# Kernel optimization log

Measured on AMD Instinct MI355X. Metric: run time of the kernel, lower is better.

Reference implementation:

```python
import jax, jax.numpy as jnp
import numpy as np

N = 8192          # rays
S = 128           # steps per ray (cfg.n_steps_fixed)
POS_BANDS = 10    # positional-encoding bands for positions
VD_BANDS = 4      # bands for view directions (default in _encode_viewdir)
EARLY_STOP_T = 1e-4


def pos_enc(x, num_bands):
    """[..., 3] -> [..., 3 + 2*3*num_bands], interleaved [x, sin(f*x), cos(f*x), ...]."""
    parts = [x]
    for i in range(num_bands):  # small fixed loop over frequency bands
        f = jnp.asarray(2.0 ** i, dtype=x.dtype)
        parts.append(jnp.sin(f * x))
        parts.append(jnp.cos(f * x))
    return jnp.concatenate(parts, axis=-1)


def setup_inputs() -> dict:
    key = jax.random.key(0)
    ks = jax.random.split(key, 10)
    orig = 0.1 * jax.random.normal(ks[0], (N, 3), jnp.float32)
    dirs = jax.random.normal(ks[1], (N, 3), jnp.float32)
    dirs = dirs / (jnp.linalg.norm(dirs, axis=-1, keepdims=True) + 1e-8)
    tmin = 0.5 + 0.5 * jax.random.uniform(ks[2], (N,), jnp.float32)
    tmax = tmin + 1.0 + jax.random.uniform(ks[3], (N,), jnp.float32)
    d_enc = 3 + 2 * 3 * POS_BANDS          # 63
    d_vd = 3 + 2 * 3 * VD_BANDS            # 27
    hid, feat = 64, 15
    W1 = jax.random.normal(ks[4], (d_enc, hid), jnp.float32) / np.sqrt(d_enc)
    b1 = jnp.zeros((hid,), jnp.float32)
    W2 = jax.random.normal(ks[5], (hid, 1 + feat), jnp.float32) / np.sqrt(hid)
    b2 = jnp.zeros((1 + feat,), jnp.float32)
    V1 = jax.random.normal(ks[6], (feat + d_vd, hid), jnp.float32) / np.sqrt(feat + d_vd)
    c1 = jnp.zeros((hid,), jnp.float32)
    V2 = jax.random.normal(ks[7], (hid, 3), jnp.float32) / np.sqrt(hid)
    c2 = jnp.zeros((3,), jnp.float32)
    return {"orig": orig, "dirs": dirs, "tmin": tmin, "tmax": tmax,
            "W1": W1, "b1": b1, "W2": W2, "b2": b2,
            "V1": V1, "c1": c1, "V2": V2, "c2": c2}


def reference(orig, dirs, tmin, tmax, W1, b1, W2, b2, V1, c1, V2, c2):
    # --- fixed-step sampling ---
    t_uniform = jnp.linspace(0.0, 1.0, S, dtype=jnp.float32)          # [S]
    t = tmin[:, None] + t_uniform[None, :] * (tmax - tmin)[:, None]   # [N, S]
    dt = jnp.mean(tmax - tmin) / S                                    # scalar step size

    # --- positions and encoder ---
    pos = orig[:, None, :] + dirs[:, None, :] * t[..., None]          # [N, S, 3]
    enc = pos_enc(pos, POS_BANDS)                                     # [N, S, 63]

    # --- field MLP: sigma + rgb features ---
    h = jax.nn.relu(enc @ W1 + b1)                                    # [N, S, 64]
    out = h @ W2 + b2                                                 # [N, S, 16]
    sigma = jax.nn.relu(out[..., 0])                                  # [N, S]
    rgb_feat = out[..., 1:]                                           # [N, S, 15]

    # --- rgb head with view-direction PE ---
    vd = dirs / (jnp.linalg.norm(dirs, axis=-1, keepdims=True) + 1e-8)
    vd_enc = pos_enc(vd, VD_BANDS)                                    # [N, 27]
    vd_enc = jnp.broadcast_to(vd_enc[:, None, :], (rgb_feat.shape[0], S, vd_enc.shape[-1]))
    rgb_in = jnp.concatenate([rgb_feat, vd_enc], axis=-1)             # [N, S, 42]
    rgb_steps = jax.nn.sigmoid(jax.nn.relu(rgb_in @ V1 + c1) @ V2 + c2)  # [N, S, 3]

    # --- alpha compositing with early stop (dense-masked equivalent) ---
    alpha = 1.0 - jnp.exp(-sigma * dt)                                # [N, S]
    one_minus = 1.0 - alpha
    T_excl = jnp.concatenate(
        [jnp.ones_like(alpha[:, :1]), jnp.cumprod(one_minus, axis=1)[:, :-1]], axis=1
    )                                                                 # transmittance before each step
    active = T_excl > EARLY_STOP_T                                    # ray still marching
    weights = T_excl * alpha * active                                 # [N, S]
    rgb_out = jnp.sum(weights[..., None] * rgb_steps, axis=1)         # [N, 3]
    T_out = jnp.prod(jnp.where(active, one_minus, 1.0), axis=1)       # final transmittance at stop
    return rgb_out, T_out
```

## Files before the change

kernel.cpp:

```cpp
#include <hip/hip_runtime.h>
#include <hip/hip_bf16.h>

#define NRAYS 8192
#define SAMP  128
#define DVD   27
#define NFEAT 15

typedef float  f32x4  __attribute__((ext_vector_type(4)));
typedef short  short8 __attribute__((ext_vector_type(8)));
typedef unsigned int u32x2 __attribute__((ext_vector_type(2)));
typedef unsigned int u32x4 __attribute__((ext_vector_type(4)));

#define GVC_OFF  16896
#define IMG_CHUNKS 1056

static __device__ __forceinline__ int XB(int row, int cb) {
    return row * 128 + (cb ^ ((row & 7) << 4));
}
static __device__ __forceinline__ int XS(int row, int k) {
    return row * 64 + (k ^ ((row & 7) << 3));
}

static __device__ __forceinline__ void stbf(short* p, float x) {
    union { unsigned u; struct { short lo, hi; } s; } v;
    v.u = __float_as_uint(x) + 0x8000u;
    *p = v.s.hi;
}
static __device__ __forceinline__ float bf2f(short s) {
    return __uint_as_float(((unsigned)(unsigned short)s) << 16);
}
static __device__ __forceinline__ unsigned pk2bf(float lo, float hi) {
    unsigned r;
    asm("v_cvt_pk_bf16_f32 %0, %1, %2" : "=v"(r) : "v"(lo), "v"(hi));
    return r;
}
static __device__ __forceinline__ float sin_fast(float x) {
    float r = x * 0.15915494309189535f;
    r = r - floorf(r);
    return __builtin_amdgcn_sinf(r);
}
static __device__ __forceinline__ float cos_fast(float x) {
    float r = x * 0.15915494309189535f;
    r = r - floorf(r);
    return __builtin_amdgcn_cosf(r);
}
static __device__ __forceinline__ float sigm(float x) {
    return 1.0f / (1.0f + __expf(-x));
}

static __device__ __forceinline__ int kmap(int r) {
    if (r == 0) return 30;
    if (r == 1) return 31;
    if (r == 2) return 62;
    const int q = r - 3, i = q / 6, c = q - 6 * i;
    return (i < 5 ? 6 * i : 32 + 6 * (i - 5)) + c;
}

__global__ void __launch_bounds__(256)
prep_kernel(const float* __restrict__ W1, const float* __restrict__ b1,
            const float* __restrict__ W2, const float* __restrict__ b2,
            const float* __restrict__ V1, const float* __restrict__ c1,
            const float* __restrict__ V2, short* __restrict__ img,
            float* __restrict__ gvc) {
    const int g = blockIdx.x * 256 + threadIdx.x;
    if (g < 4032) {
        const int r = g >> 6, n = g & 63;
        const int prow = (n & 3) * 16 + (n >> 2);
        stbf(&img[XS(prow, kmap(r))], W1[g]);
    } else if (g < 4096) {
        const int n = g - 4032;
        const int prow = (n & 3) * 16 + (n >> 2);
        stbf(&img[XS(prow, 63)], b1[n]);
    } else if (g < 8192) {
        const int i = g - 4096;
        const int k = i >> 6, n = i & 63;
        const int prow = (n & 3) * 16 + (n >> 2);
        float a = 0.0f;
        #pragma unroll
        for (int j = 0; j < 15; j++) a += W2[k * 16 + 1 + j] * V1[j * 64 + n];
        stbf(&img[4096 + XS(prow, k)], a);
    } else if (g < 8256) {
        const int k = g - 8192;
        stbf(&img[8192 + k], W2[k * 16]);
    } else if (g < 8448) {
        const int i = g - 8256, c = i >> 6, k = i & 63;
        stbf(&img[8192 + 64 + c * 64 + k], V2[k * 3 + c]);
    } else if (g < 8512) {
        const int n = g - 8448;
        float a = c1[n];
        #pragma unroll
        for (int j = 0; j < 15; j++) a += b2[1 + j] * V1[j * 64 + n];
        gvc[n] = a;
    }
}

#define SMEM_BYTES 38400

__global__ void __launch_bounds__(256, 4)
march_kernel(const float* __restrict__ orig,
             const float* __restrict__ dirs,
             const float* __restrict__ tmin,
             const float* __restrict__ tmax,
             const float* __restrict__ b2,
             const float* __restrict__ c2,
             const float* __restrict__ V1,
             const short* __restrict__ img,
             const float* __restrict__ gvc,
             float* __restrict__ out) {
    __shared__ __align__(16) char smem[SMEM_BYTES];
    char*  const sEc   = smem;
    char*  const sW1tc = smem + 16384;
    char*  const sCtc  = smem + 24576;
    short* const sSm   = (short*)(smem + 32768);
    float* const sOm   = (float*)(smem + 33280);
    short* const sRgb  = (short*)(smem + 35328);
    float* const sVde  = (float*)(smem);
    float* const sRed  = (float*)(smem + 448);

    const int tid  = threadIdx.x;
    const int lane = tid & 63;
    const int wave = tid >> 6;
    const int ray  = blockIdx.x * 4 + wave;

    {
        const float4* tm0 = (const float4*)tmin;
        const float4* tm1 = (const float4*)tmax;
        float s = 0.0f;
        #pragma unroll
        for (int it = 0; it < 8; it++) {
            const int i = tid + it * 256;
            const float4 a = tm1[i], b = tm0[i];
            s += (a.x - b.x) + (a.y - b.y) + (a.z - b.z) + (a.w - b.w);
        }
        #pragma unroll
        for (int off = 32; off > 0; off >>= 1)
            s += __shfl_xor(s, off, 64);
        if (lane == 0) sRed[wave] = s;
    }

    {
        const u32x4* src = (const u32x4*)img;
        u32x4* dst = (u32x4*)(smem + 16384);
        #pragma unroll
        for (int it = 0; it < 5; it++) {
            const int i = tid + it * 256;
            if (i < IMG_CHUNKS) dst[i] = src[i];
        }
    }

    const float ox = orig[ray * 3 + 0];
    const float oy = orig[ray * 3 + 1];
    const float oz = orig[ray * 3 + 2];
    const float dx = dirs[ray * 3 + 0];
    const float dy = dirs[ray * 3 + 1];
    const float dz = dirs[ray * 3 + 2];
    const float t0v = tmin[ray];
    const float trange = tmax[ray] - t0v;

    {
        const float nrm = sqrtf(dx * dx + dy * dy + dz * dz);
        const float inv = 1.0f / (nrm + 1e-8f);
        const float vx = dx * inv, vy = dy * inv, vz = dz * inv;
        if (lane < DVD) {
            float val;
            if (lane < 3) {
                val = (lane == 0) ? vx : ((lane == 1) ? vy : vz);
            } else {
                const int q = lane - 3;
                const int b = q / 6;
                const int r = q - 6 * b;
                const bool isSin = (r < 3);
                const int d = isSin ? r : (r - 3);
                const float comp = (d == 0) ? vx : ((d == 1) ? vy : vz);
                const float a = (float)(1 << b) * comp;
                val = isSin ? sin_fast(a) : cos_fast(a);
            }
            sVde[wave * 28 + lane] = val;
        }
    }
    __syncthreads();

    const float dtv = (sRed[0] + sRed[1] + sRed[2] + sRed[3]) *
                      (1.0f / ((float)NRAYS * (float)SAMP));
    const float negdtv = -dtv;

    const int nfr  = lane & 15;
    const int quad = lane >> 4;
    const int cbq  = quad * 16;

    float gv[4];
    {
        const f32x4 g0 = *(const f32x4*)&gvc[4 * nfr];
        gv[0] = g0.x; gv[1] = g0.y; gv[2] = g0.z; gv[3] = g0.w;
    }
    #pragma unroll 9
    for (int q = 0; q < DVD; q++) {
        const float e = sVde[wave * 28 + q];
        const f32x4 vv = *(const f32x4*)&V1[(NFEAT + q) * 64 + 4 * nfr];
        gv[0] += e * vv.x; gv[1] += e * vv.y;
        gv[2] += e * vv.z; gv[3] += e * vv.w;
    }

    const float bb2 = b2[0];
    const float bc2 = (nfr < 3) ? c2[nfr] : 0.0f;

    __syncthreads();

    char* const myE = sEc + wave * 4096;

    const int sl   = lane >> 1;
    const int half = lane & 1;
    const float fmul = half ? 5.0929581789406507f
                            : 0.15915494309189535f;

    #pragma unroll 1
    for (int qq = 0; qq < 4; qq++) {
        {
            const int s = qq * 32 + sl;
            const float t = t0v + (float)s * (1.0f / 127.0f) * trange;
            const float px = ox + dx * t, py = oy + dy * t, pz = oz + dz * t;
            float rx = px * fmul; rx -= floorf(rx);
            float ry = py * fmul; ry -= floorf(ry);
            float rz = pz * fmul; rz -= floorf(rz);
            float sx = __builtin_amdgcn_sinf(rx), cx = __builtin_amdgcn_cosf(rx);
            float sy = __builtin_amdgcn_sinf(ry), cy = __builtin_amdgcn_cosf(ry);
            float sz = __builtin_amdgcn_sinf(rz), cz = __builtin_amdgcn_cosf(rz);
            unsigned e[16] __attribute__((aligned(16)));
            #pragma unroll
            for (int j = 0; j < 5; j++) {
                e[3 * j + 0] = pk2bf(sx, sy);
                e[3 * j + 1] = pk2bf(sz, cx);
                e[3 * j + 2] = pk2bf(cy, cz);
                if (j < 4) {
                    const float tx = sx + sx, ty = sy + sy, tz = sz + sz;
                    const float nsx = tx * cx, nsy = ty * cy, nsz = tz * cz;
                    cx = __builtin_fmaf(-tx, sx, 1.0f);
                    cy = __builtin_fmaf(-ty, sy, 1.0f);
                    cz = __builtin_fmaf(-tz, sz, 1.0f);
                    sx = nsx; sy = nsy; sz = nsz;
                }
            }
            e[15] = half ? pk2bf(pz, 1.0f) : pk2bf(px, py);
            #pragma unroll
            for (int w = 0; w < 4; w++)
                *(u32x4*)(myE + XB(sl, half * 64 + w * 16)) =
                    *(const u32x4*)&e[4 * w];
        }
        f32x4 acc1[2][4];
        {
            short8 af[2][2];
            #pragma unroll
            for (int mt = 0; mt < 2; mt++)
                #pragma unroll
                for (int kt = 0; kt < 2; kt++)
                    af[mt][kt] = *(const short8*)(myE + XB(nfr + 16 * mt, cbq + kt * 64));
            __builtin_amdgcn_s_setprio(1);
            #pragma unroll
            for (int nt = 0; nt < 4; nt++) {
                const short8 wf0 = *(const short8*)
                    (sW1tc + XB(nt * 16 + nfr, cbq));
                #pragma unroll
                for (int mt = 0; mt < 2; mt++)
                    acc1[mt][nt] = __builtin_amdgcn_mfma_f32_16x16x32_bf16(
                        af[mt][0], wf0, (f32x4){0.0f, 0.0f, 0.0f, 0.0f}, 0, 0, 0);
                const short8 wf1 = *(const short8*)
                    (sW1tc + XB(nt * 16 + nfr, cbq + 64));
                #pragma unroll
                for (int mt = 0; mt < 2; mt++)
                    acc1[mt][nt] = __builtin_amdgcn_mfma_f32_16x16x32_bf16(
                        af[mt][1], wf1, acc1[mt][nt], 0, 0, 0);
            }
            __builtin_amdgcn_s_setprio(0);
        }
        #pragma unroll
        for (int mt = 0; mt < 2; mt++)
            #pragma unroll
            for (int r = 0; r < 4; r++) {
                const int m = 4 * quad + r + 16 * mt;
                u32x2 hp;
                hp.x = pk2bf(fmaxf(acc1[mt][0][r], 0.0f),
                             fmaxf(acc1[mt][1][r], 0.0f));
                hp.y = pk2bf(fmaxf(acc1[mt][2][r], 0.0f),
                             fmaxf(acc1[mt][3][r], 0.0f));
                *(u32x2*)(myE + XB(m, 8 * nfr)) = hp;
            }
        short8 ah[2][2];
        #pragma unroll
        for (int mt = 0; mt < 2; mt++)
            #pragma unroll
            for (int kt = 0; kt < 2; kt++)
                ah[mt][kt] = *(const short8*)(myE + XB(nfr + 16 * mt, cbq + kt * 64));
        {
            f32x4 acc2[2];
            acc2[0] = (f32x4){bb2, bb2, bb2, bb2};
            acc2[1] = (f32x4){bb2, bb2, bb2, bb2};
            short8 w2sf[2];
            #pragma unroll
            for (int kt = 0; kt < 2; kt++)
                w2sf[kt] = *(const short8*)&sSm[quad * 8 + kt * 32];
            __builtin_amdgcn_s_setprio(1);
            #pragma unroll
            for (int mt = 0; mt < 2; mt++)
                #pragma unroll
                for (int kt = 0; kt < 2; kt++)
                    acc2[mt] = __builtin_amdgcn_mfma_f32_16x16x32_bf16(
                        ah[mt][kt], w2sf[kt], acc2[mt], 0, 0, 0);
            __builtin_amdgcn_s_setprio(0);
            if (nfr == 0) {
                #pragma unroll
                for (int mt = 0; mt < 2; mt++)
                    #pragma unroll
                    for (int r = 0; r < 4; r++) {
                        const int m = 4 * quad + r + 16 * mt;
                        sOm[wave * 128 + qq * 32 + m] =
                            fmaxf(acc2[mt][r], 0.0f) * negdtv;
                    }
            }
        }
        #pragma unroll
        for (int nth = 0; nth < 2; nth++) {
            f32x4 acc3[2][2];
            #pragma unroll
            for (int mt = 0; mt < 2; mt++)
                #pragma unroll
                for (int j = 0; j < 2; j++) {
                    const float gvi = gv[2 * nth + j];
                    acc3[mt][j] = (f32x4){gvi, gvi, gvi, gvi};
                }
            __builtin_amdgcn_s_setprio(1);
            #pragma unroll
            for (int j = 0; j < 2; j++)
                #pragma unroll
                for (int kt = 0; kt < 2; kt++) {
                    const short8 cf = *(const short8*)
                        (sCtc + XB((2 * nth + j) * 16 + nfr, cbq + kt * 64));
                    #pragma unroll
                    for (int mt = 0; mt < 2; mt++)
                        acc3[mt][j] = __builtin_amdgcn_mfma_f32_16x16x32_bf16(
                            ah[mt][kt], cf, acc3[mt][j], 0, 0, 0);
                }
            __builtin_amdgcn_s_setprio(0);
            #pragma unroll
            for (int mt = 0; mt < 2; mt++)
                #pragma unroll
                for (int r = 0; r < 4; r++) {
                    const int m = 4 * quad + r + 16 * mt;
                    *(unsigned*)(myE + XB(m, 8 * nfr + 4 * nth)) =
                        pk2bf(fmaxf(acc3[mt][0][r], 0.0f),
                              fmaxf(acc3[mt][1][r], 0.0f));
                }
        }
        {
            f32x4 acc4[2];
            acc4[0] = (f32x4){bc2, bc2, bc2, bc2};
            acc4[1] = (f32x4){bc2, bc2, bc2, bc2};
            short8 agg[2][2];
            #pragma unroll
            for (int mt = 0; mt < 2; mt++)
                #pragma unroll
                for (int kt = 0; kt < 2; kt++)
                    agg[mt][kt] = *(const short8*)(myE + XB(nfr + 16 * mt, cbq + kt * 64));
            const int vr = 1 + ((nfr < 3) ? nfr : 2);
            short8 v2f[2];
            #pragma unroll
            for (int kt = 0; kt < 2; kt++)
                v2f[kt] = *(const short8*)&sSm[vr * 64 + quad * 8 + kt * 32];
            __builtin_amdgcn_s_setprio(1);
            #pragma unroll
            for (int mt = 0; mt < 2; mt++)
                #pragma unroll
                for (int kt = 0; kt < 2; kt++)
                    acc4[mt] = __builtin_amdgcn_mfma_f32_16x16x32_bf16(
                        agg[mt][kt], v2f[kt], acc4[mt], 0, 0, 0);
            __builtin_amdgcn_s_setprio(0);
            if (nfr < 3) {
                #pragma unroll
                for (int mt = 0; mt < 2; mt++)
                    #pragma unroll
                    for (int r = 0; r < 4; r++) {
                        const int m = 4 * quad + r + 16 * mt;
                        stbf(&sRgb[wave * 384 + (qq * 32 + m) * 3 + nfr],
                             acc4[mt][r]);
                    }
            }
        }
    }

    const float om0 = __expf(sOm[wave * 128 + 2 * lane]);
    const float om1 = __expf(sOm[wave * 128 + 2 * lane + 1]);
    const float al0 = 1.0f - om0;
    const float al1 = 1.0f - om1;

    float inc = om0 * om1;
    #pragma unroll
    for (int off = 1; off < 64; off <<= 1) {
        const float q = __shfl_up(inc, off, 64);
        if (lane >= off) inc *= q;
    }
    float Texc = __shfl_up(inc, 1, 64);
    if (lane == 0) Texc = 1.0f;

    const float T0 = Texc;
    const float T1 = Texc * om0;
    const float a0 = (T0 > 1e-4f) ? 1.0f : 0.0f;
    const float a1 = (T1 > 1e-4f) ? 1.0f : 0.0f;
    const float w0 = T0 * al0 * a0;
    const float w1 = T1 * al1 * a1;

    float cr = w0 * sigm(bf2f(sRgb[wave * 384 + (2 * lane) * 3 + 0])) +
               w1 * sigm(bf2f(sRgb[wave * 384 + (2 * lane + 1) * 3 + 0]));
    float cg = w0 * sigm(bf2f(sRgb[wave * 384 + (2 * lane) * 3 + 1])) +
               w1 * sigm(bf2f(sRgb[wave * 384 + (2 * lane + 1) * 3 + 1]));
    float cb = w0 * sigm(bf2f(sRgb[wave * 384 + (2 * lane) * 3 + 2])) +
               w1 * sigm(bf2f(sRgb[wave * 384 + (2 * lane + 1) * 3 + 2]));
    float tp = (a0 > 0.0f ? om0 : 1.0f) * (a1 > 0.0f ? om1 : 1.0f);

    #pragma unroll
    for (int off = 32; off > 0; off >>= 1) {
        cr += __shfl_xor(cr, off, 64);
        cg += __shfl_xor(cg, off, 64);
        cb += __shfl_xor(cb, off, 64);
        tp *= __shfl_xor(tp, off, 64);
    }

    if (lane == 0) {
        out[ray * 3 + 0] = cr;
        out[ray * 3 + 1] = cg;
        out[ray * 3 + 2] = cb;
        out[NRAYS * 3 + ray] = tp;
    }
}

extern "C" void kernel_launch(void* const* d_in, const int* in_sizes, int n_in,
                              void* d_out, int out_size, void* d_ws, size_t ws_size,
                              hipStream_t stream) {
    const float* orig = (const float*)d_in[0];
    const float* dirs = (const float*)d_in[1];
    const float* tmin = (const float*)d_in[2];
    const float* tmax = (const float*)d_in[3];
    const float* W1   = (const float*)d_in[4];
    const float* b1   = (const float*)d_in[5];
    const float* W2   = (const float*)d_in[6];
    const float* b2   = (const float*)d_in[7];
    const float* V1   = (const float*)d_in[8];
    const float* c1   = (const float*)d_in[9];
    const float* V2   = (const float*)d_in[10];
    const float* c2   = (const float*)d_in[11];

    short* img = (short*)d_ws;
    float* gvc = (float*)((char*)d_ws + GVC_OFF);

    prep_kernel<<<34, 256, 0, stream>>>(W1, b1, W2, b2, V1, c1, V2, img, gvc);
    march_kernel<<<NRAYS / 4, 256, 0, stream>>>(orig, dirs, tmin, tmax,
                                                b2, c2, V1, img, gvc,
                                                (float*)d_out);
}
```

Measured before the change: 115.0 us.

## Precompute dt in prep kernel and software-pipeline positional encoding across chunks

The global mean step size is now reduced once by an extra prep-kernel block and written to the workspace, so the 2048 march blocks no longer each re-read all of tmin/tmax. The positional encoding for the next 32-sample chunk is computed during the current chunk, after the third MLP layer, so transcendental ALU work can overlap MFMA work. The first-layer MFMA is split into two halves to reduce accumulator register pressure. The cost is that the encoded values stay live across the loop, and the last iteration computes one chunk that is never used.

Result: no change. 115.2 us (+0.1%).

```diff
diff --git a/kernel.cpp b/kernel.cpp
--- a/kernel.cpp
+++ b/kernel.cpp
@@ -56,12 +56,64 @@
     return (i < 5 ? 6 * i : 32 + 6 * (i - 5)) + c;
 }
 
+static __device__ __forceinline__ void enc_compute(
+    int s, float t0v, float trange,
+    float ox, float oy, float oz, float dx, float dy, float dz,
+    float fmul, int half, unsigned* e) {
+    const float t = t0v + (float)s * (1.0f / 127.0f) * trange;
+    const float px = ox + dx * t, py = oy + dy * t, pz = oz + dz * t;
+    float rx = px * fmul; rx -= floorf(rx);
+    float ry = py * fmul; ry -= floorf(ry);
+    float rz = pz * fmul; rz -= floorf(rz);
+    float sx = __builtin_amdgcn_sinf(rx), cx = __builtin_amdgcn_cosf(rx);
+    float sy = __builtin_amdgcn_sinf(ry), cy = __builtin_amdgcn_cosf(ry);
+    float sz = __builtin_amdgcn_sinf(rz), cz = __builtin_amdgcn_cosf(rz);
+    #pragma unroll
+    for (int j = 0; j < 5; j++) {
+        e[3 * j + 0] = pk2bf(sx, sy);
+        e[3 * j + 1] = pk2bf(sz, cx);
+        e[3 * j + 2] = pk2bf(cy, cz);
+        if (j < 4) {
+            const float tx = sx + sx, ty = sy + sy, tz = sz + sz;
+            const float nsx = tx * cx, nsy = ty * cy, nsz = tz * cz;
+            cx = __builtin_fmaf(-tx, sx, 1.0f);
+            cy = __builtin_fmaf(-ty, sy, 1.0f);
+            cz = __builtin_fmaf(-tz, sz, 1.0f);
+            sx = nsx; sy = nsy; sz = nsz;
+        }
+    }
+    e[15] = half ? pk2bf(pz, 1.0f) : pk2bf(px, py);
+}
+
 __global__ void __launch_bounds__(256)
 prep_kernel(const float* __restrict__ W1, const float* __restrict__ b1,
             const float* __restrict__ W2, const float* __restrict__ b2,
             const float* __restrict__ V1, const float* __restrict__ c1,
-            const float* __restrict__ V2, short* __restrict__ img,
+            const float* __restrict__ V2, const float* __restrict__ tmin,
+            const float* __restrict__ tmax, short* __restrict__ img,
             float* __restrict__ gvc) {
+    if (blockIdx.x == 34) {
+        __shared__ float red[4];
+        const int tid = threadIdx.x, lane = tid & 63, wave = tid >> 6;
+        const float4* tm0 = (const float4*)tmin;
+        const float4* tm1 = (const float4*)tmax;
+        float s = 0.0f;
+        #pragma unroll
+        for (int it = 0; it < 8; it++) {
+            const int i = tid + it * 256;
+            const float4 a = tm1[i], b = tm0[i];
+            s += (a.x - b.x) + (a.y - b.y) + (a.z - b.z) + (a.w - b.w);
+        }
+        #pragma unroll
+        for (int off = 32; off > 0; off >>= 1)
+            s += __shfl_xor(s, off, 64);
+        if (lane == 0) red[wave] = s;
+        __syncthreads();
+        if (tid == 0)
+            gvc[64] = (red[0] + red[1] + red[2] + red[3]) *
+                      (1.0f / ((float)NRAYS * (float)SAMP));
+        return;
+    }
     const int g = blockIdx.x * 256 + threadIdx.x;
     if (g < 4032) {
         const int r = g >> 6, n = g & 63;
@@ -115,28 +167,11 @@
     float* const sOm   = (float*)(smem + 33280);
     short* const sRgb  = (short*)(smem + 35328);
     float* const sVde  = (float*)(smem);
-    float* const sRed  = (float*)(smem + 448);
 
     const int tid  = threadIdx.x;
     const int lane = tid & 63;
     const int wave = tid >> 6;
     const int ray  = blockIdx.x * 4 + wave;
-
-    {
-        const float4* tm0 = (const float4*)tmin;
-        const float4* tm1 = (const float4*)tmax;
-        float s = 0.0f;
-        #pragma unroll
-        for (int it = 0; it < 8; it++) {
-            const int i = tid + it * 256;
-            const float4 a = tm1[i], b = tm0[i];
-            s += (a.x - b.x) + (a.y - b.y) + (a.z - b.z) + (a.w - b.w);
-        }
-        #pragma unroll
-        for (int off = 32; off > 0; off >>= 1)
-            s += __shfl_xor(s, off, 64);
-        if (lane == 0) sRed[wave] = s;
-    }
 
     {
         const u32x4* src = (const u32x4*)img;
@@ -156,6 +191,7 @@
     const float dz = dirs[ray * 3 + 2];
     const float t0v = tmin[ray];
     const float trange = tmax[ray] - t0v;
+    const float negdtv = -gvc[64];
 
     {
         const float nrm = sqrtf(dx * dx + dy * dy + dz * dz);
@@ -180,10 +216,6 @@
     }
     __syncthreads();
 
-    const float dtv = (sRed[0] + sRed[1] + sRed[2] + sRed[3]) *
-                      (1.0f / ((float)NRAYS * (float)SAMP));
-    const float negdtv = -dtv;
-
     const int nfr  = lane & 15;
     const int quad = lane >> 4;
     const int cbq  = quad * 16;
@@ -213,40 +245,15 @@
     const float fmul = half ? 5.0929581789406507f
                             : 0.15915494309189535f;
 
+    unsigned e[16] __attribute__((aligned(16)));
+    enc_compute(sl, t0v, trange, ox, oy, oz, dx, dy, dz, fmul, half, e);
+
     #pragma unroll 1
     for (int qq = 0; qq < 4; qq++) {
-        {
-            const int s = qq * 32 + sl;
-            const float t = t0v + (float)s * (1.0f / 127.0f) * trange;
-            const float px = ox + dx * t, py = oy + dy * t, pz = oz + dz * t;
-            float rx = px * fmul; rx -= floorf(rx);
-            float ry = py * fmul; ry -= floorf(ry);
-            float rz = pz * fmul; rz -= floorf(rz);
-            float sx = __builtin_amdgcn_sinf(rx), cx = __builtin_amdgcn_cosf(rx);
-            float sy = __builtin_amdgcn_sinf(ry), cy = __builtin_amdgcn_cosf(ry);
-            float sz = __builtin_amdgcn_sinf(rz), cz = __builtin_amdgcn_cosf(rz);
-            unsigned e[16] __attribute__((aligned(16)));
-            #pragma unroll
-            for (int j = 0; j < 5; j++) {
-                e[3 * j + 0] = pk2bf(sx, sy);
-                e[3 * j + 1] = pk2bf(sz, cx);
-                e[3 * j + 2] = pk2bf(cy, cz);
-                if (j < 4) {
-                    const float tx = sx + sx, ty = sy + sy, tz = sz + sz;
-                    const float nsx = tx * cx, nsy = ty * cy, nsz = tz * cz;
-                    cx = __builtin_fmaf(-tx, sx, 1.0f);
-                    cy = __builtin_fmaf(-ty, sy, 1.0f);
-                    cz = __builtin_fmaf(-tz, sz, 1.0f);
-                    sx = nsx; sy = nsy; sz = nsz;
-                }
-            }
-            e[15] = half ? pk2bf(pz, 1.0f) : pk2bf(px, py);
-            #pragma unroll
-            for (int w = 0; w < 4; w++)
-                *(u32x4*)(myE + XB(sl, half * 64 + w * 16)) =
-                    *(const u32x4*)&e[4 * w];
-        }
-        f32x4 acc1[2][4];
+        #pragma unroll
+        for (int w = 0; w < 4; w++)
+            *(u32x4*)(myE + XB(sl, half * 64 + w * 16)) =
+                *(const u32x4*)&e[4 * w];
         {
             short8 af[2][2];
             #pragma unroll
@@ -254,36 +261,38 @@
                 #pragma unroll
                 for (int kt = 0; kt < 2; kt++)
                     af[mt][kt] = *(const short8*)(myE + XB(nfr + 16 * mt, cbq + kt * 64));
-            __builtin_amdgcn_s_setprio(1);
-            #pragma unroll
-            for (int nt = 0; nt < 4; nt++) {
-                const short8 wf0 = *(const short8*)
-                    (sW1tc + XB(nt * 16 + nfr, cbq));
+            #pragma unroll
+            for (int nth = 0; nth < 2; nth++) {
+                f32x4 acc1[2][2];
+                __builtin_amdgcn_s_setprio(1);
+                #pragma unroll
+                for (int j = 0; j < 2; j++) {
+                    const int nt = 2 * nth + j;
+                    const short8 wf0 = *(const short8*)
+                        (sW1tc + XB(nt * 16 + nfr, cbq));
+                    #pragma unroll
+                    for (int mt = 0; mt < 2; mt++)
+                        acc1[mt][j] = __builtin_amdgcn_mfma_f32_16x16x32_bf16(
+                            af[mt][0], wf0, (f32x4){0.0f, 0.0f, 0.0f, 0.0f}, 0, 0, 0);
+                    const short8 wf1 = *(const short8*)
+                        (sW1tc + XB(nt * 16 + nfr, cbq + 64));
+                    #pragma unroll
+                    for (int mt = 0; mt < 2; mt++)
+                        acc1[mt][j] = __builtin_amdgcn_mfma_f32_16x16x32_bf16(
+                            af[mt][1], wf1, acc1[mt][j], 0, 0, 0);
+                }
+                __builtin_amdgcn_s_setprio(0);
                 #pragma unroll
                 for (int mt = 0; mt < 2; mt++)
-                    acc1[mt][nt] = __builtin_amdgcn_mfma_f32_16x16x32_bf16(
-                        af[mt][0], wf0, (f32x4){0.0f, 0.0f, 0.0f, 0.0f}, 0, 0, 0);
-                const short8 wf1 = *(const short8*)
-                    (sW1tc + XB(nt * 16 + nfr, cbq + 64));
-                #pragma unroll
-                for (int mt = 0; mt < 2; mt++)
-                    acc1[mt][nt] = __builtin_amdgcn_mfma_f32_16x16x32_bf16(
-                        af[mt][1], wf1, acc1[mt][nt], 0, 0, 0);
+                    #pragma unroll
+                    for (int r = 0; r < 4; r++) {
+                        const int m = 4 * quad + r + 16 * mt;
+                        *(unsigned*)(myE + XB(m, 8 * nfr + 4 * nth)) =
+                            pk2bf(fmaxf(acc1[mt][0][r], 0.0f),
+                                  fmaxf(acc1[mt][1][r], 0.0f));
+                    }
             }
-            __builtin_amdgcn_s_setprio(0);
-        }
-        #pragma unroll
-        for (int mt = 0; mt < 2; mt++)
-            #pragma unroll
-            for (int r = 0; r < 4; r++) {
-                const int m = 4 * quad + r + 16 * mt;
-                u32x2 hp;
-                hp.x = pk2bf(fmaxf(acc1[mt][0][r], 0.0f),
-                             fmaxf(acc1[mt][1][r], 0.0f));
-                hp.y = pk2bf(fmaxf(acc1[mt][2][r], 0.0f),
-                             fmaxf(acc1[mt][3][r], 0.0f));
-                *(u32x2*)(myE + XB(m, 8 * nfr)) = hp;
-            }
+        }
         short8 ah[2][2];
         #pragma unroll
         for (int mt = 0; mt < 2; mt++)
@@ -350,6 +359,8 @@
                               fmaxf(acc3[mt][1][r], 0.0f));
                 }
         }
+        enc_compute((qq + 1) * 32 + sl, t0v, trange, ox, oy, oz, dx, dy, dz,
+                    fmul, half, e);
         {
             f32x4 acc4[2];
             acc4[0] = (f32x4){bc2, bc2, bc2, bc2};
@@ -450,7 +461,8 @@
     short* img = (short*)d_ws;
     float* gvc = (float*)((char*)d_ws + GVC_OFF);
 
-    prep_kernel<<<34, 256, 0, stream>>>(W1, b1, W2, b2, V1, c1, V2, img, gvc);
+    prep_kernel<<<35, 256, 0, stream>>>(W1, b1, W2, b2, V1, c1, V2,
+                                        tmin, tmax, img, gvc);
     march_kernel<<<NRAYS / 4, 256, 0, stream>>>(orig, dirs, tmin, tmax,
                                                 b2, c2, V1, img, gvc,
                                                 (float*)d_out);
```
